# Optimization experiments

Measured on AMD Instinct MI355X. Metric: run time of the kernel, lower is better.

## Reference

```python
import jax, jax.numpy as jnp
import numpy as np

N_NODES = 50000
N_GRAPHS = 64
HID = 100

def gcn_conv(x, W, b, src, dst, n):
    # dense transform first (PyG GCNConv): [N, out]
    h = x @ W
    # add self loops (improved=False -> fill 1.0)
    loops = jnp.arange(n, dtype=src.dtype)
    s = jnp.concatenate([src, loops])
    d = jnp.concatenate([dst, loops])
    # symmetric normalization D^-1/2 A D^-1/2
    deg = jax.ops.segment_sum(jnp.ones_like(s, dtype=h.dtype), d, num_segments=n)
    dinv = jnp.where(deg > 0, jax.lax.rsqrt(jnp.maximum(deg, 1e-12)), 0.0)
    norm = dinv[s] * dinv[d]  # [E+N]
    msgs = h[s] * norm[:, None]  # gather + scale
    out = jax.ops.segment_sum(msgs, d, num_segments=n)  # scatter-add
    return out + b

def global_mean_pool(x, batch, num_graphs):
    sums = jax.ops.segment_sum(x, batch, num_segments=num_graphs)
    cnts = jax.ops.segment_sum(jnp.ones((x.shape[0],), x.dtype), batch, num_segments=num_graphs)
    return sums / jnp.maximum(cnts, 1.0)[:, None]

def setup_inputs() -> dict:
    key = jax.random.key(0)
    ks = jax.random.split(key, 8)
    d_in = 128
    x = jax.random.normal(ks[0], (N_NODES, d_in), dtype=jnp.float32)
    edge_index = jax.random.randint(ks[1], (2, 800000), 0, N_NODES, dtype=jnp.int64)
    batch = jnp.sort(jax.random.randint(ks[2], (N_NODES,), 0, N_GRAPHS, dtype=jnp.int64))
    s1 = 1.0 / np.sqrt(d_in)
    s2 = 1.0 / np.sqrt(HID)
    W1 = jax.random.uniform(ks[3], (d_in, HID), jnp.float32, -s1, s1)
    b1 = jnp.zeros((HID,), jnp.float32)
    W2 = jax.random.uniform(ks[4], (HID, HID), jnp.float32, -s2, s2)
    b2 = jnp.zeros((HID,), jnp.float32)
    Wlin = jax.random.uniform(ks[5], (HID, 1), jnp.float32, -s2, s2)
    blin = jax.random.uniform(ks[6], (1,), jnp.float32, -s2, s2)
    return {"x": x, "edge_index": edge_index, "batch": batch,
            "W1": W1, "b1": b1, "W2": W2, "b2": b2, "Wlin": Wlin, "blin": blin}

def reference(x, edge_index, batch, W1, b1, W2, b2, Wlin, blin):
    src, dst = edge_index[0], edge_index[1]
    h = gcn_conv(x, W1, b1, src, dst, N_NODES)
    h = jnp.tanh(h)
    h = gcn_conv(h, W2, b2, src, dst, N_NODES)
    g = global_mean_pool(h, batch, N_GRAPHS)  # [G, HID]
    return g @ Wlin + blin  # [G, 1]
```

## Files before the change

kernel.cpp:

```cpp
#include <hip/hip_runtime.h>
#include <hip/hip_bf16.h>

#define N_NODES 50000
#define N_GRAPHS 64
#define HID 100
#define HP 104

#define BKE  4096
#define NBIN 196
#define CAP  8192
#define NPB 39

#define OFF_DINV 0
#define OFF_CNTF 50048
#define OFF_POOL 50112
#define OFF_WT1  50176
#define OFF_HS   64512
#define OFF_ROWPTR 2664512
#define OFF_DEG    2714560
#define OFF_EIDX   2739648
#define OFF_BE     3542464
#define OFF_CURSOR 5148096
#define OFF_DONE   5148352
#define OFF_W2L    5148416
#define OFF_Q      5148544

typedef __attribute__((ext_vector_type(8))) short short8;
typedef __attribute__((ext_vector_type(4))) float floatx4;

__device__ inline float b2f(unsigned int u) {
    union { unsigned int v; float f; } x; x.v = u << 16; return x.f;
}
__device__ inline unsigned short f2b(float f) {
    union { float f; unsigned int v; } x; x.f = f;
    unsigned int r = (x.v + 0x7fffu + ((x.v >> 16) & 1u)) >> 16;
    return (unsigned short)r;
}

__global__ __launch_bounds__(256) void k_prep(const float* __restrict__ W1,
                                              const float* __restrict__ W2,
                                              const float* __restrict__ Wlin,
                                              const float* __restrict__ b2,
                                              unsigned short* __restrict__ Wt1,
                                              float* __restrict__ w2l,
                                              float* __restrict__ pool,
                                              float* __restrict__ cntf,
                                              int* __restrict__ done,
                                              int* __restrict__ cursor) {
    const int b = blockIdx.x, t = threadIdx.x;
    if (b < 56) {
        int idx = b * 256 + t;
        int c = idx >> 7, k = idx & 127;
        float v = (k < 128 && c < HID) ? W1[k * HID + c] : 0.0f;
        Wt1[c * 128 + k] = f2b(v);
    } else if (b == 56) {
        if (t < 104) {
            float s = 0.0f;
            if (t < 100)
                for (int c = 0; c < HID; ++c) s += W2[t * HID + c] * Wlin[c];
            w2l[t] = s;
        } else if (t == 104) {
            float s = 0.0f;
            for (int j = 0; j < HID; ++j) s += b2[j] * Wlin[j];
            w2l[104] = s;
        } else if (t >= 128 && t < 128 + N_GRAPHS) {
            pool[t - 128] = 0.0f; cntf[t - 128] = 0.0f;
        } else if (t == 224) {
            *done = 0;
        }
    } else {
        if (t < NBIN) cursor[t] = 0;
    }
}

__global__ __launch_bounds__(256) void k_sort(const int* __restrict__ src,
                                              const int* __restrict__ dst, int E,
                                              int* __restrict__ cursor,
                                              unsigned int* __restrict__ bE) {
    __shared__ unsigned int stage[BKE];
    __shared__ int hist[256], pref[256], cur[256], sb[256], resS[256];
    const int t = threadIdx.x, b = blockIdx.x;
    hist[t] = 0;
    __syncthreads();
    const int e0 = b * BKE, e1 = min(e0 + BKE, E), n = e1 - e0;
    unsigned int mine[16];
#pragma unroll
    for (int u = 0; u < 16; ++u) {
        int e = e0 + u * 256 + t;
        if (e < e1) {
            unsigned int v = ((unsigned int)src[e] << 16) | (unsigned int)dst[e];
            mine[u] = v;
            atomicAdd(&hist[(v >> 8) & 255], 1);
        }
    }
    __syncthreads();
    sb[t] = hist[t];
    __syncthreads();
    for (int off = 1; off < 256; off <<= 1) {
        int v = (t >= off) ? sb[t - off] : 0;
        __syncthreads();
        sb[t] += v;
        __syncthreads();
    }
    pref[t] = sb[t] - hist[t];
    cur[t] = pref[t];
    if (t < NBIN && hist[t] > 0) resS[t] = atomicAdd(&cursor[t], hist[t]);
    __syncthreads();
#pragma unroll
    for (int u = 0; u < 16; ++u) {
        int e = e0 + u * 256 + t;
        if (e < e1) {
            unsigned int v = mine[u];
            int p = atomicAdd(&cur[(v >> 8) & 255], 1);
            stage[p] = v;
        }
    }
    __syncthreads();
    for (int i = t; i < n; i += 256) {
        unsigned int v = stage[i];
        int bin = (v >> 8) & 255;
        int rel = resS[bin] + (i - pref[bin]);
        if (rel < CAP) bE[bin * CAP + rel] = v;
    }
}

__global__ __launch_bounds__(256) void k_p4(const unsigned int* __restrict__ bE,
                                            const int* __restrict__ cursor,
                                            int* __restrict__ rowptr,
                                            unsigned short* __restrict__ deg,
                                            unsigned short* __restrict__ eidx,
                                            float* __restrict__ dinv) {
    __shared__ int hist[256], pref[256], cur[256], sb[256];
    const int t = threadIdx.x, b = blockIdx.x;
    const int eBase = b * CAP;
    int n = cursor[b];
    if (n > CAP) n = CAP;
    hist[t] = 0;
    __syncthreads();
    for (int i = t; i < n; i += 256) atomicAdd(&hist[bE[eBase + i] & 255], 1);
    __syncthreads();
    sb[t] = hist[t];
    __syncthreads();
    for (int off = 1; off < 256; off <<= 1) {
        int v = (t >= off) ? sb[t - off] : 0;
        __syncthreads();
        sb[t] += v;
        __syncthreads();
    }
    pref[t] = sb[t] - hist[t];
    cur[t] = pref[t];
    int node = (b << 8) + t;
    if (node < N_NODES) {
        rowptr[node] = eBase + pref[t];
        deg[node] = (unsigned short)hist[t];
        dinv[node] = rsqrtf((float)(hist[t] + 1));
    }
    __syncthreads();
    for (int i = t; i < n; i += 256) {
        unsigned int v = bE[eBase + i];
        int p = atomicAdd(&cur[v & 255], 1);
        eidx[eBase + p] = (unsigned short)(v >> 16);
    }
}

__global__ __launch_bounds__(256) void k_gemm(const float* __restrict__ A,
                                              const unsigned short* __restrict__ Wt,
                                              const float* __restrict__ dinv,
                                              unsigned short* __restrict__ out) {
    __shared__ __align__(16) unsigned short xs[64][136];
    __shared__ __align__(16) unsigned short ws[112][136];
    const int t = threadIdx.x;
    const int base = blockIdx.x * 64;

    for (int idx = t; idx < 112 * 64; idx += 256) {
        int c = idx >> 6, u = idx & 63;
        *(unsigned int*)&ws[c][2 * u] = ((const unsigned int*)Wt)[idx];
    }
    for (int idx = t; idx < 64 * 32; idx += 256) {
        int r = idx >> 5, q = idx & 31;
        int row = base + r;
        ushort4 p;
        if (row < N_NODES) {
            float4 v = ((const float4*)(A + (size_t)row * 128))[q];
            p.x = f2b(v.x); p.y = f2b(v.y); p.z = f2b(v.z); p.w = f2b(v.w);
        } else p = make_ushort4(0, 0, 0, 0);
        *(ushort4*)&xs[r][4 * q] = p;
    }
    __syncthreads();

    const int lane = t & 63, w = t >> 6;
    const int g = lane >> 4, cl = lane & 15;

    floatx4 acc[7];
#pragma unroll
    for (int n = 0; n < 7; ++n) acc[n] = (floatx4){0.f, 0.f, 0.f, 0.f};

#pragma unroll
    for (int kc = 0; kc < 4; ++kc) {
        short8 a = *(const short8*)&xs[w * 16 + cl][kc * 32 + 8 * g];
#pragma unroll
        for (int n = 0; n < 7; ++n) {
            short8 b = *(const short8*)&ws[n * 16 + cl][kc * 32 + 8 * g];
            acc[n] = __builtin_amdgcn_mfma_f32_16x16x32_bf16(a, b, acc[n], 0, 0, 0);
        }
    }

    float di[4]; int lrows[4];
#pragma unroll
    for (int r = 0; r < 4; ++r) {
        lrows[r] = w * 16 + 4 * g + r;
        int grow = base + lrows[r];
        di[r] = (grow < N_NODES) ? dinv[grow] : 0.0f;
    }
#pragma unroll
    for (int n = 0; n < 7; ++n) {
        int col = n * 16 + cl;
#pragma unroll
        for (int r = 0; r < 4; ++r)
            xs[lrows[r]][col] = f2b(acc[n][r] * di[r]);
    }
    __syncthreads();
    for (int idx = t; idx < 64 * 13; idx += 256) {
        int r = idx / 13, q = idx - r * 13;
        int row = base + r;
        if (row < N_NODES)
            *(uint4*)(out + (size_t)row * HP + 8 * q) = *(const uint4*)&xs[r][8 * q];
    }
}

#define ACC8(v) do { \
    s[0] += b2f((v).x & 0xffff); s[1] += b2f((v).x >> 16); \
    s[2] += b2f((v).y & 0xffff); s[3] += b2f((v).y >> 16); \
    s[4] += b2f((v).z & 0xffff); s[5] += b2f((v).z >> 16); \
    s[6] += b2f((v).w & 0xffff); s[7] += b2f((v).w >> 16); } while (0)

__global__ __launch_bounds__(512) void k_gather_q(const int* __restrict__ rowptr,
                                                  const unsigned short* __restrict__ deg,
                                                  const unsigned short* __restrict__ eidx,
                                                  const unsigned short* __restrict__ hs,
                                                  const float* __restrict__ dinv,
                                                  const float* __restrict__ b1,
                                                  const float* __restrict__ w2l,
                                                  float* __restrict__ q) {
    __shared__ float wl[104];
    __shared__ float bsh[104];
    __shared__ float part[512];
    const int t = threadIdx.x;
    if (t < 104) { wl[t] = w2l[t]; bsh[t] = (t < 100) ? b1[t] : 0.0f; }
    const int nid = t / 13, c = t - nid * 13;
    const int i = blockIdx.x * NPB + nid;
    const bool active = (t < NPB * 13) && (i < N_NODES);
    __syncthreads();

    float partial = 0.0f;
    float di = 0.0f;
    if (active) {
        const int c0 = 8 * c;
        float s[8] = {0.f, 0.f, 0.f, 0.f, 0.f, 0.f, 0.f, 0.f};
        uint4 sv = *(const uint4*)(hs + (size_t)i * HP + c0);
        ACC8(sv);
        int e = rowptr[i];
        const int end = e + deg[i];
        for (; e + 16 <= end; e += 16) {
            int n[16];
#pragma unroll
            for (int u = 0; u < 16; ++u) n[u] = eidx[e + u];
            uint4 v[16];
#pragma unroll
            for (int u = 0; u < 16; ++u) v[u] = *(const uint4*)(hs + (size_t)n[u] * HP + c0);
#pragma unroll
            for (int u = 0; u < 16; ++u) ACC8(v[u]);
        }
        for (; e + 8 <= end; e += 8) {
            int n[8];
#pragma unroll
            for (int u = 0; u < 8; ++u) n[u] = eidx[e + u];
            uint4 v[8];
#pragma unroll
            for (int u = 0; u < 8; ++u) v[u] = *(const uint4*)(hs + (size_t)n[u] * HP + c0);
#pragma unroll
            for (int u = 0; u < 8; ++u) ACC8(v[u]);
        }
        for (; e + 4 <= end; e += 4) {
            int n[4];
#pragma unroll
            for (int u = 0; u < 4; ++u) n[u] = eidx[e + u];
            uint4 v[4];
#pragma unroll
            for (int u = 0; u < 4; ++u) v[u] = *(const uint4*)(hs + (size_t)n[u] * HP + c0);
#pragma unroll
            for (int u = 0; u < 4; ++u) ACC8(v[u]);
        }
        for (; e < end; ++e) {
            uint4 v = *(const uint4*)(hs + (size_t)eidx[e] * HP + c0);
            ACC8(v);
        }
        di = dinv[i];
#pragma unroll
        for (int j = 0; j < 8; ++j) {
            float h = tanhf(di * s[j] + bsh[c0 + j]);
            partial += h * wl[c0 + j];
        }
    }
    part[t] = partial;
    __syncthreads();
    if (active && c == 0) {
        float sum = 0.0f;
#pragma unroll
        for (int j = 0; j < 13; ++j) sum += part[t + j];
        q[i] = di * sum;
    }
}

__global__ __launch_bounds__(256) void k_gpool(const int* __restrict__ rowptr,
                                               const unsigned short* __restrict__ deg,
                                               const unsigned short* __restrict__ eidx,
                                               const float* __restrict__ q,
                                               const float* __restrict__ dinv,
                                               const int* __restrict__ batch,
                                               float* __restrict__ pool,
                                               float* __restrict__ cntf,
                                               const float* __restrict__ w2l,
                                               const float* __restrict__ blin,
                                               int* __restrict__ done,
                                               float* __restrict__ out) {
    __shared__ float sp[N_GRAPHS];
    __shared__ float sc[N_GRAPHS];
    __shared__ int lastFlag;
    const int t = threadIdx.x;
    if (t < N_GRAPHS) { sp[t] = 0.0f; sc[t] = 0.0f; }
    __syncthreads();
    int i = blockIdx.x * 256 + t;
    if (i < N_NODES) {
        float s = q[i];
        int e = rowptr[i];
        const int end = e + deg[i];
        for (; e + 8 <= end; e += 8) {
            int n0 = eidx[e],     n1 = eidx[e + 1], n2 = eidx[e + 2], n3 = eidx[e + 3];
            int n4 = eidx[e + 4], n5 = eidx[e + 5], n6 = eidx[e + 6], n7 = eidx[e + 7];
            s += q[n0] + q[n1] + q[n2] + q[n3] + q[n4] + q[n5] + q[n6] + q[n7];
        }
        for (; e + 4 <= end; e += 4) {
            int n0 = eidx[e], n1 = eidx[e + 1], n2 = eidx[e + 2], n3 = eidx[e + 3];
            s += q[n0] + q[n1] + q[n2] + q[n3];
        }
        for (; e < end; ++e) s += q[eidx[e]];
        float p = dinv[i] * s;
        int g = batch[i];
        atomicAdd(&sp[g], p);
        atomicAdd(&sc[g], 1.0f);
    }
    __syncthreads();
    if (t < N_GRAPHS && (sp[t] != 0.0f || sc[t] != 0.0f)) {
        atomicAdd(&pool[t], sp[t]);
        atomicAdd(&cntf[t], sc[t]);
    }
    __syncthreads();
    if (t == 0) {
        __threadfence();
        int ticket = atomicAdd(done, 1);
        lastFlag = (ticket == (int)gridDim.x - 1);
    }
    __syncthreads();
    if (lastFlag && t < N_GRAPHS) {
        float p = atomicAdd(&pool[t], 0.0f);
        float c = atomicAdd(&cntf[t], 0.0f);
        out[t] = p / fmaxf(c, 1.0f) + w2l[104] + blin[0];
    }
}

extern "C" void kernel_launch(void* const* d_in, const int* in_sizes, int n_in,
                              void* d_out, int out_size, void* d_ws, size_t ws_size,
                              hipStream_t stream) {
    const float* x    = (const float*)d_in[0];
    const int*   ei   = (const int*)d_in[1];
    const int*   batch= (const int*)d_in[2];
    const float* W1   = (const float*)d_in[3];
    const float* b1   = (const float*)d_in[4];
    const float* W2   = (const float*)d_in[5];
    const float* b2   = (const float*)d_in[6];
    const float* Wlin = (const float*)d_in[7];
    const float* blin = (const float*)d_in[8];
    float* out = (float*)d_out;

    const int E = in_sizes[1] / 2;
    const int* src = ei;
    const int* dst = ei + E;

    float* wsf  = (float*)d_ws;
    int*   wsi  = (int*)d_ws;
    float* dinv = wsf + OFF_DINV;
    float* cntf = wsf + OFF_CNTF;
    float* pool = wsf + OFF_POOL;
    unsigned short* Wt1 = (unsigned short*)(wsf + OFF_WT1);
    unsigned short* HS  = (unsigned short*)(wsf + OFF_HS);
    int* rowptr = wsi + OFF_ROWPTR;
    unsigned short* deg  = (unsigned short*)(wsi + OFF_DEG);
    unsigned short* eidx = (unsigned short*)(wsi + OFF_EIDX);
    unsigned int* bE = (unsigned int*)(wsi + OFF_BE);
    int* cursor = wsi + OFF_CURSOR;
    int* done   = wsi + OFF_DONE;
    float* w2l  = wsf + OFF_W2L;
    float* q    = wsf + OFF_Q;

    const int nbE = (E + BKE - 1) / BKE;
    const int nGrid = (N_NODES + 255) / 256;
    const int gqGrid = (N_NODES + NPB - 1) / NPB;

    k_prep<<<58, 256, 0, stream>>>(W1, W2, Wlin, b2, Wt1, w2l, pool, cntf, done, cursor);
    k_sort<<<nbE, 256, 0, stream>>>(src, dst, E, cursor, bE);
    k_p4<<<NBIN, 256, 0, stream>>>(bE, cursor, rowptr, deg, eidx, dinv);

    k_gemm<<<(N_NODES + 63) / 64, 256, 0, stream>>>(x, Wt1, dinv, HS);

    k_gather_q<<<gqGrid, 512, 0, stream>>>(rowptr, deg, eidx, HS, dinv, b1, w2l, q);

    k_gpool<<<nGrid, 256, 0, stream>>>(rowptr, deg, eidx, q, dinv, batch, pool, cntf,
                                       w2l, blin, done, out);
}
```

Measured before the change: 96.63 us.

## Store transformed node features as custom 8-bit float to halve gather traffic

The first-layer transformed features are now encoded as a custom sign plus 7-bit exponent/mantissa byte format (an e4m3-like scaled encoding) instead of bf16. Rows are padded to 112 bytes, so each neighbour gather reads 7 lanes of 16 bytes rather than 13 lanes of 16 bytes. Nodes per block in the gather kernel rise to fit the new lane count, and the 16-wide unrolled edge loop is dropped. This targets the memory bandwidth of the random neighbour gather, but the 8-bit encoding loses precision and range (it clamps large values), which could affect accuracy, and the decode costs extra ALU work.

```diff
diff --git a/kernel.cpp b/kernel.cpp
--- a/kernel.cpp
+++ b/kernel.cpp
@@ -4,37 +4,52 @@
 #define N_NODES 50000
 #define N_GRAPHS 64
 #define HID 100
-#define HP 104
+#define HPB 112
 
 #define BKE  4096
 #define NBIN 196
 #define CAP  8192
-#define NPB 39
+#define NPB 73
 
 #define OFF_DINV 0
 #define OFF_CNTF 50048
 #define OFF_POOL 50112
 #define OFF_WT1  50176
-#define OFF_HS   64512
-#define OFF_ROWPTR 2664512
-#define OFF_DEG    2714560
-#define OFF_EIDX   2739648
-#define OFF_BE     3542464
-#define OFF_CURSOR 5148096
-#define OFF_DONE   5148352
-#define OFF_W2L    5148416
-#define OFF_Q      5148544
+#define OFF_HS   57344
+#define OFF_ROWPTR 1457344
+#define OFF_DEG    1507392
+#define OFF_EIDX   1532480
+#define OFF_BE     2335296
+#define OFF_CURSOR 3940928
+#define OFF_DONE   3941184
+#define OFF_W2L    3941248
+#define OFF_Q      3941376
 
 typedef __attribute__((ext_vector_type(8))) short short8;
 typedef __attribute__((ext_vector_type(4))) float floatx4;
 
-__device__ inline float b2f(unsigned int u) {
-    union { unsigned int v; float f; } x; x.v = u << 16; return x.f;
-}
 __device__ inline unsigned short f2b(float f) {
     union { float f; unsigned int v; } x; x.f = f;
     unsigned int r = (x.v + 0x7fffu + ((x.v >> 16) & 1u)) >> 16;
     return (unsigned short)r;
+}
+
+__device__ inline unsigned int f2e(float f) {
+    float a = fabsf(f) * 0x1.0p-114f;
+    a = fminf(a, 0x1.Cp-112f);
+    unsigned int u = __float_as_uint(a);
+    unsigned int b = (u + 0x7FFFFu + ((u >> 20) & 1u)) >> 20;
+    return b | ((__float_as_uint(f) >> 24) & 0x80u);
+}
+__device__ inline float e2f(unsigned int b) {
+    return __uint_as_float(((b << 24) & 0x80000000u) | ((b & 0x7Fu) << 20)) * 0x1.0p114f;
+}
+__device__ inline void acc16(float* s, uint4 v) {
+    unsigned int x;
+    x = v.x; s[0]  += e2f(x); s[1]  += e2f(x >> 8); s[2]  += e2f(x >> 16); s[3]  += e2f(x >> 24);
+    x = v.y; s[4]  += e2f(x); s[5]  += e2f(x >> 8); s[6]  += e2f(x >> 16); s[7]  += e2f(x >> 24);
+    x = v.z; s[8]  += e2f(x); s[9]  += e2f(x >> 8); s[10] += e2f(x >> 16); s[11] += e2f(x >> 24);
+    x = v.w; s[12] += e2f(x); s[13] += e2f(x >> 8); s[14] += e2f(x >> 16); s[15] += e2f(x >> 24);
 }
 
 __global__ __launch_bounds__(256) void k_prep(const float* __restrict__ W1,
@@ -54,15 +69,15 @@
         float v = (k < 128 && c < HID) ? W1[k * HID + c] : 0.0f;
         Wt1[c * 128 + k] = f2b(v);
     } else if (b == 56) {
-        if (t < 104) {
+        if (t < 112) {
             float s = 0.0f;
             if (t < 100)
                 for (int c = 0; c < HID; ++c) s += W2[t * HID + c] * Wlin[c];
             w2l[t] = s;
-        } else if (t == 104) {
+        } else if (t == 112) {
             float s = 0.0f;
             for (int j = 0; j < HID; ++j) s += b2[j] * Wlin[j];
-            w2l[104] = s;
+            w2l[112] = s;
         } else if (t >= 128 && t < 128 + N_GRAPHS) {
             pool[t - 128] = 0.0f; cntf[t - 128] = 0.0f;
         } else if (t == 224) {
@@ -166,7 +181,7 @@
 __global__ __launch_bounds__(256) void k_gemm(const float* __restrict__ A,
                                               const unsigned short* __restrict__ Wt,
                                               const float* __restrict__ dinv,
-                                              unsigned short* __restrict__ out) {
+                                              unsigned char* __restrict__ out) {
     __shared__ __align__(16) unsigned short xs[64][136];
     __shared__ __align__(16) unsigned short ws[112][136];
     const int t = threadIdx.x;
@@ -212,74 +227,62 @@
         int grow = base + lrows[r];
         di[r] = (grow < N_NODES) ? dinv[grow] : 0.0f;
     }
+    __syncthreads();
+    unsigned char* os = (unsigned char*)&xs[0][0];
 #pragma unroll
     for (int n = 0; n < 7; ++n) {
         int col = n * 16 + cl;
 #pragma unroll
         for (int r = 0; r < 4; ++r)
-            xs[lrows[r]][col] = f2b(acc[n][r] * di[r]);
-    }
-    __syncthreads();
-    for (int idx = t; idx < 64 * 13; idx += 256) {
-        int r = idx / 13, q = idx - r * 13;
+            os[lrows[r] * HPB + col] = (unsigned char)f2e(acc[n][r] * di[r]);
+    }
+    __syncthreads();
+    for (int idx = t; idx < 64 * 7; idx += 256) {
+        int r = idx / 7, q = idx - r * 7;
         int row = base + r;
         if (row < N_NODES)
-            *(uint4*)(out + (size_t)row * HP + 8 * q) = *(const uint4*)&xs[r][8 * q];
-    }
-}
-
-#define ACC8(v) do { \
-    s[0] += b2f((v).x & 0xffff); s[1] += b2f((v).x >> 16); \
-    s[2] += b2f((v).y & 0xffff); s[3] += b2f((v).y >> 16); \
-    s[4] += b2f((v).z & 0xffff); s[5] += b2f((v).z >> 16); \
-    s[6] += b2f((v).w & 0xffff); s[7] += b2f((v).w >> 16); } while (0)
+            *(uint4*)(out + (size_t)row * HPB + 16 * q) = *(const uint4*)(os + r * HPB + 16 * q);
+    }
+}
 
 __global__ __launch_bounds__(512) void k_gather_q(const int* __restrict__ rowptr,
                                                   const unsigned short* __restrict__ deg,
                                                   const unsigned short* __restrict__ eidx,
-                                                  const unsigned short* __restrict__ hs,
+                                                  const unsigned char* __restrict__ hs,
                                                   const float* __restrict__ dinv,
                                                   const float* __restrict__ b1,
                                                   const float* __restrict__ w2l,
                                                   float* __restrict__ q) {
-    __shared__ float wl[104];
-    __shared__ float bsh[104];
+    __shared__ float wl[112];
+    __shared__ float bsh[112];
     __shared__ float part[512];
     const int t = threadIdx.x;
-    if (t < 104) { wl[t] = w2l[t]; bsh[t] = (t < 100) ? b1[t] : 0.0f; }
-    const int nid = t / 13, c = t - nid * 13;
+    if (t < 112) { wl[t] = w2l[t]; bsh[t] = (t < 100) ? b1[t] : 0.0f; }
+    const int nid = t / 7, c = t - nid * 7;
     const int i = blockIdx.x * NPB + nid;
-    const bool active = (t < NPB * 13) && (i < N_NODES);
+    const bool active = (t < NPB * 7) && (i < N_NODES);
     __syncthreads();
 
     float partial = 0.0f;
     float di = 0.0f;
     if (active) {
-        const int c0 = 8 * c;
-        float s[8] = {0.f, 0.f, 0.f, 0.f, 0.f, 0.f, 0.f, 0.f};
-        uint4 sv = *(const uint4*)(hs + (size_t)i * HP + c0);
-        ACC8(sv);
+        const int c0 = 16 * c;
+        float s[16];
+#pragma unroll
+        for (int j = 0; j < 16; ++j) s[j] = 0.0f;
+        uint4 sv = *(const uint4*)(hs + (size_t)i * HPB + c0);
+        acc16(s, sv);
         int e = rowptr[i];
         const int end = e + deg[i];
-        for (; e + 16 <= end; e += 16) {
-            int n[16];
-#pragma unroll
-            for (int u = 0; u < 16; ++u) n[u] = eidx[e + u];
-            uint4 v[16];
-#pragma unroll
-            for (int u = 0; u < 16; ++u) v[u] = *(const uint4*)(hs + (size_t)n[u] * HP + c0);
-#pragma unroll
-            for (int u = 0; u < 16; ++u) ACC8(v[u]);
-        }
         for (; e + 8 <= end; e += 8) {
             int n[8];
 #pragma unroll
             for (int u = 0; u < 8; ++u) n[u] = eidx[e + u];
             uint4 v[8];
 #pragma unroll
-            for (int u = 0; u < 8; ++u) v[u] = *(const uint4*)(hs + (size_t)n[u] * HP + c0);
-#pragma unroll
-            for (int u = 0; u < 8; ++u) ACC8(v[u]);
+            for (int u = 0; u < 8; ++u) v[u] = *(const uint4*)(hs + (size_t)n[u] * HPB + c0);
+#pragma unroll
+            for (int u = 0; u < 8; ++u) acc16(s, v[u]);
         }
         for (; e + 4 <= end; e += 4) {
             int n[4];
@@ -287,17 +290,17 @@
             for (int u = 0; u < 4; ++u) n[u] = eidx[e + u];
             uint4 v[4];
 #pragma unroll
-            for (int u = 0; u < 4; ++u) v[u] = *(const uint4*)(hs + (size_t)n[u] * HP + c0);
-#pragma unroll
-            for (int u = 0; u < 4; ++u) ACC8(v[u]);
+            for (int u = 0; u < 4; ++u) v[u] = *(const uint4*)(hs + (size_t)n[u] * HPB + c0);
+#pragma unroll
+            for (int u = 0; u < 4; ++u) acc16(s, v[u]);
         }
         for (; e < end; ++e) {
-            uint4 v = *(const uint4*)(hs + (size_t)eidx[e] * HP + c0);
-            ACC8(v);
+            uint4 v = *(const uint4*)(hs + (size_t)eidx[e] * HPB + c0);
+            acc16(s, v);
         }
         di = dinv[i];
 #pragma unroll
-        for (int j = 0; j < 8; ++j) {
+        for (int j = 0; j < 16; ++j) {
             float h = tanhf(di * s[j] + bsh[c0 + j]);
             partial += h * wl[c0 + j];
         }
@@ -307,7 +310,7 @@
     if (active && c == 0) {
         float sum = 0.0f;
 #pragma unroll
-        for (int j = 0; j < 13; ++j) sum += part[t + j];
+        for (int j = 0; j < 7; ++j) sum += part[t + j];
         q[i] = di * sum;
     }
 }
@@ -365,7 +368,7 @@
     if (lastFlag && t < N_GRAPHS) {
         float p = atomicAdd(&pool[t], 0.0f);
         float c = atomicAdd(&cntf[t], 0.0f);
-        out[t] = p / fmaxf(c, 1.0f) + w2l[104] + blin[0];
+        out[t] = p / fmaxf(c, 1.0f) + w2l[112] + blin[0];
     }
 }
 
@@ -393,7 +396,7 @@
     float* cntf = wsf + OFF_CNTF;
     float* pool = wsf + OFF_POOL;
     unsigned short* Wt1 = (unsigned short*)(wsf + OFF_WT1);
-    unsigned short* HS  = (unsigned short*)(wsf + OFF_HS);
+    unsigned char*  HS  = (unsigned char*)(wsf + OFF_HS);
     int* rowptr = wsi + OFF_ROWPTR;
     unsigned short* deg  = (unsigned short*)(wsi + OFF_DEG);
     unsigned short* eidx = (unsigned short*)(wsi + OFF_EIDX);
```

Measured after the change: 107.9 us. +11.7%, slower.
